# Optimization experiments

Measured on AMD Instinct MI355X. Metric: run time of the kernel, lower is better.

The kernel has to match this reference:

```python
import jax, jax.numpy as jnp
import numpy as np
from jax import lax

B, L, C, K = 32, 128, 192, 3


def conv1d_same(x, w, b):
    # x: [B, L, C], w: [K, Cin, Cout], b: [Cout]
    y = lax.conv_general_dilated(x, w, window_strides=(1,), padding='SAME',
                                 dimension_numbers=('NWC', 'WIO', 'NWC'))
    return y + b


def shift_right(x):
    # ShiftLayer: shift memory one step along length axis, zero-padded
    return jnp.pad(x, ((0, 0), (1, 0), (0, 0)))[:, :-1, :]


def setup_inputs() -> dict:
    key = jax.random.key(0)
    ks = jax.random.split(key, 4)
    scale = 1.0 / np.sqrt(K * C)
    x = jax.random.normal(ks[0], (B, L, C), dtype=jnp.float32)
    w_reset = jax.random.normal(ks[1], (K, C, C), dtype=jnp.float32) * scale
    w_gate = jax.random.normal(ks[2], (K, C, C), dtype=jnp.float32) * scale
    w_cand = jax.random.normal(ks[3], (K, C, C), dtype=jnp.float32) * scale
    b_reset = jnp.full((C,), 0.5, dtype=jnp.float32)  # bias_initializer 0.5
    b_gate = jnp.full((C,), 0.7, dtype=jnp.float32)   # bias_initializer 0.7
    b_cand = jnp.zeros((C,), dtype=jnp.float32)       # bias_initializer 0.0
    return {'x': x, 'w_reset': w_reset, 'b_reset': b_reset,
            'w_gate': w_gate, 'b_gate': b_gate,
            'w_cand': w_cand, 'b_cand': b_cand}


def reference(x, w_reset, b_reset, w_gate, b_gate, w_cand, b_cand):
    def step(mem, _):
        shifted = shift_right(mem)
        reset = jax.nn.sigmoid(conv1d_same(mem, w_reset, b_reset))
        gate = jax.nn.sigmoid(conv1d_same(mem, w_gate, b_gate))
        cand = jnp.tanh(conv1d_same(reset * mem, w_cand, b_cand))
        out = gate * shifted + (1.0 - gate) * cand
        return out, None

    # DNGPU unrolls the gated-conv cell for `length` (= seq_len) steps
    out, _ = lax.scan(step, x, None, length=L)
    return out
```

## Files before the change

### kernel.cpp

```cpp
#include <hip/hip_runtime.h>

typedef __attribute__((ext_vector_type(8))) short short8;
typedef __attribute__((ext_vector_type(4))) float f32x4;

#define NROWS 4096
#define CC    192
#define NCEL  (NROWS * CC)

#define W1ELEM (4 * 18 * 96 * 32)
#define W2ELEM (2 * 18 * 96 * 32)

typedef const __attribute__((address_space(1))) void as1_void;
typedef __attribute__((address_space(3))) void as3_void;
#define GLD_LDS16(G, L) __builtin_amdgcn_global_load_lds((as1_void*)(G), (as3_void*)(L), 16, 0, 0)

__device__ __forceinline__ unsigned short f2bf(float x) {
    union { float f; unsigned int u; } v; v.f = x;
    unsigned int r = v.u + 0x7fffu + ((v.u >> 16) & 1u);
    return (unsigned short)(r >> 16);
}
__device__ __forceinline__ float bf2f(unsigned short h) {
    union { unsigned int u; float f; } v; v.u = ((unsigned int)h) << 16;
    return v.f;
}
__device__ __forceinline__ unsigned packhl(float x) {
    unsigned short h = f2bf(x);
    unsigned short l = f2bf(x - bf2f(h));
    return (unsigned)h | ((unsigned)l << 16);
}
__device__ __forceinline__ float unpackhl(unsigned v) {
    return bf2f((unsigned short)(v & 0xFFFFu)) + bf2f((unsigned short)(v >> 16));
}
__device__ __forceinline__ float sigmoid_f(float x) {
    return 1.0f / (1.0f + __expf(-x));
}
__device__ __forceinline__ float tanh_f(float x) {
    float ax = fabsf(x);
    if (ax < 0.0625f) {
        float x2 = x * x;
        return x * fmaf(x2, fmaf(x2, 0.13333333f, -0.33333333f), 1.0f);
    }
    float e = __expf(2.0f * fminf(ax, 20.0f));
    float t = (e - 1.0f) / (e + 1.0f);
    return x < 0.0f ? -t : t;
}

__global__ void prep_x(const float* __restrict__ x, unsigned* __restrict__ memHL) {
    int i = blockIdx.x * 256 + threadIdx.x;
    if (i < NCEL) memHL[i] = packhl(x[i]);
}

__global__ void prep_w(const float* __restrict__ wr, const float* __restrict__ wg,
                       const float* __restrict__ wc,
                       unsigned short* __restrict__ W1H, unsigned short* __restrict__ W1L,
                       unsigned short* __restrict__ W2H, unsigned short* __restrict__ W2L) {
    int i = blockIdx.x * 256 + threadIdx.x;
    if (i >= W1ELEM + W2ELEM) return;
    const float* w; int grp, rem, cbase; unsigned short *H, *L; int dst;
    if (i < W1ELEM) {
        grp = i / 55296; rem = i % 55296;
        w = (grp >> 1) ? wg : wr;
        cbase = (grp & 1) * 96;
        H = W1H; L = W1L; dst = i;
    } else {
        int ii = i - W1ELEM;
        grp = ii / 55296; rem = ii % 55296;
        w = wc; cbase = grp * 96;
        H = W2H; L = W2L; dst = ii;
    }
    int ch = rem / 3072, r2 = rem % 3072, col = r2 / 32, kc = r2 % 32;
    int kk = ch / 6, ci = (ch % 6) * 32 + kc;
    int c = cbase + col;
    float v = w[(size_t)(kk * 192 + ci) * 192 + c];
    unsigned short h = f2bf(v);
    H[dst] = h; L[dst] = f2bf(v - bf2f(h));
}

#define ASTAGE(SRC, NT, NIT) do {                                                    \
    _Pragma("unroll")                                                                \
    for (int it_ = 0; it_ < (NIT); ++it_) {                                          \
        int q_ = it_ * (NT) + tid;                                                   \
        if (q_ < 34 * 96) {                                                          \
            int row_ = q_ / 96, u_ = q_ - row_ * 96;                                 \
            int gr_ = n0 - 1 + row_;                                                 \
            unsigned long long v_ = 0ull;                                            \
            if (gr_ >= 0 && ((gr_ >> 7) == (n0 >> 7)))                               \
                v_ = *(const unsigned long long*)((SRC) + (size_t)gr_ * 192 + u_ * 2);\
            unsigned lo_ = (unsigned)v_, hi_ = (unsigned)(v_ >> 32);                 \
            unsigned byt_ = ((unsigned)(u_ * 4)) ^ (((unsigned)(row_ & 7)) << 4);    \
            unsigned wdx_ = (((unsigned)row_) * 384 + byt_) >> 2;                    \
            ((unsigned*)AH)[wdx_] = (lo_ & 0xFFFFu) | (hi_ << 16);                   \
            ((unsigned*)AL)[wdx_] = (lo_ >> 16) | (hi_ & 0xFFFF0000u);               \
        }                                                                            \
    }                                                                                \
} while (0)

__global__ __launch_bounds__(128)
void k1_rg(const unsigned* __restrict__ mem,
           const unsigned short* __restrict__ W1H, const unsigned short* __restrict__ W1L,
           const float* __restrict__ b_r, const float* __restrict__ b_g,
           float* __restrict__ gate, unsigned* __restrict__ rm)
{
    __shared__ __align__(16) unsigned short AH[34 * 192];
    __shared__ __align__(16) unsigned short AL[34 * 192];
    __shared__ __align__(16) unsigned short WB[2][2][96 * 32];

    const int strip = blockIdx.x, grp = blockIdx.y;
    const int n0 = strip * 32;
    const int tid = threadIdx.x;

    ASTAGE(mem, 128, 26);

    const int lane = tid & 63, w = tid >> 6;
    const int lrow = lane & 15, lkg = lane >> 4;

    const unsigned short* Wp = (w ? W1L : W1H) + (size_t)grp * 55296;
    #define STAGEB1(BUF, CH) do {                                                    \
        const unsigned short* s_ = Wp + (CH) * 3072 + lane * 8;                      \
        unsigned short* d_ = &WB[BUF][w][0];                                         \
        _Pragma("unroll")                                                            \
        for (int j_ = 0; j_ < 6; ++j_)                                               \
            GLD_LDS16(s_ + j_ * 512, d_ + j_ * 512);                                 \
    } while (0)

    STAGEB1(0, 0);
    __syncthreads();

    f32x4 acc[2][3] = {};
    int buf = 0;
    #pragma unroll 2
    for (int ch = 0; ch < 18; ++ch) {
        if (ch < 17) STAGEB1(buf ^ 1, ch + 1);
        const int kk = ch / 6, cib = (ch % 6) * 32;
        short8 aH[2], aL[2];
        #pragma unroll
        for (int mt = 0; mt < 2; ++mt) {
            const int slot = 16 * mt + lrow + kk;
            const unsigned byt = ((unsigned)((cib + lkg * 8) * 2)) ^ (((unsigned)(slot & 7)) << 4);
            const int off = slot * 192 + (byt >> 1);
            aH[mt] = *(const short8*)(AH + off);
            aL[mt] = *(const short8*)(AL + off);
        }
        short8 bH[3], bL[3];
        #pragma unroll
        for (int j = 0; j < 3; ++j) {
            const int c = w * 48 + j * 16 + lrow;
            bH[j] = *(const short8*)(&WB[buf][0][c * 32 + lkg * 8]);
            bL[j] = *(const short8*)(&WB[buf][1][c * 32 + lkg * 8]);
        }
        #pragma unroll
        for (int mt = 0; mt < 2; ++mt)
            #pragma unroll
            for (int j = 0; j < 3; ++j) {
                acc[mt][j] = __builtin_amdgcn_mfma_f32_16x16x32_bf16(aH[mt], bH[j], acc[mt][j], 0, 0, 0);
                acc[mt][j] = __builtin_amdgcn_mfma_f32_16x16x32_bf16(aL[mt], bH[j], acc[mt][j], 0, 0, 0);
                acc[mt][j] = __builtin_amdgcn_mfma_f32_16x16x32_bf16(aH[mt], bL[j], acc[mt][j], 0, 0, 0);
            }
        __syncthreads();
        buf ^= 1;
    }

    const int conv = grp >> 1;
    const int c0g = (grp & 1) * 96 + w * 48;
    #pragma unroll
    for (int j = 0; j < 3; ++j) {
        const int c = c0g + 16 * j + lrow;
        const float bb = conv ? b_g[c] : b_r[c];
        #pragma unroll
        for (int mt = 0; mt < 2; ++mt) {
            #pragma unroll
            for (int r = 0; r < 4; ++r) {
                const int row = n0 + 16 * mt + lkg * 4 + r;
                const size_t idx = (size_t)row * 192 + c;
                const float s = sigmoid_f(acc[mt][j][r] + bb);
                if (conv == 0) {
                    const float m = unpackhl(mem[idx]);
                    rm[idx] = packhl(s * m);
                } else {
                    gate[idx] = s;
                }
            }
        }
    }
}

__global__ __launch_bounds__(256)
void k2_c(const unsigned* __restrict__ rm,
          const unsigned short* __restrict__ W2H, const unsigned short* __restrict__ W2L,
          const float* __restrict__ b_c, const float* __restrict__ gate,
          const unsigned* __restrict__ mem, unsigned* __restrict__ nxt,
          float* __restrict__ outF, int last)
{
    __shared__ __align__(16) unsigned short AH[34 * 192];
    __shared__ __align__(16) unsigned short AL[34 * 192];
    __shared__ __align__(16) unsigned short WB[2][2][96 * 32];

    const int strip = blockIdx.x, grp = blockIdx.y;
    const int n0 = strip * 32;
    const int tid = threadIdx.x;

    ASTAGE(rm, 256, 13);

    const int lane = tid & 63, w = tid >> 6;
    const int lrow = lane & 15, lkg = lane >> 4;
    const int mtw = w >> 1, ng = w & 1;

    const unsigned short* WpH = W2H + (size_t)grp * 55296;
    const unsigned short* WpL = W2L + (size_t)grp * 55296;
    #define STAGEB2(BUF, CH) do {                                                    \
        _Pragma("unroll")                                                            \
        for (int j_ = 0; j_ < 3; ++j_) {                                             \
            const int id_ = w * 3 + j_;                                              \
            const int pl_ = id_ / 6, sg_ = id_ % 6;                                  \
            const unsigned short* s_ = (pl_ ? WpL : WpH) + (CH) * 3072 + sg_ * 512 + lane * 8; \
            GLD_LDS16(s_, &WB[BUF][pl_][sg_ * 512]);                                 \
        }                                                                            \
    } while (0)

    STAGEB2(0, 0);
    __syncthreads();

    f32x4 acc[3] = {};
    int buf = 0;
    #pragma unroll 2
    for (int ch = 0; ch < 18; ++ch) {
        if (ch < 17) STAGEB2(buf ^ 1, ch + 1);
        const int kk = ch / 6, cib = (ch % 6) * 32;
        const int slot = 16 * mtw + lrow + kk;
        const unsigned byt = ((unsigned)((cib + lkg * 8) * 2)) ^ (((unsigned)(slot & 7)) << 4);
        const int off = slot * 192 + (byt >> 1);
        const short8 aH = *(const short8*)(AH + off);
        const short8 aL = *(const short8*)(AL + off);
        short8 bH[3], bL[3];
        #pragma unroll
        for (int j = 0; j < 3; ++j) {
            const int c = ng * 48 + j * 16 + lrow;
            bH[j] = *(const short8*)(&WB[buf][0][c * 32 + lkg * 8]);
            bL[j] = *(const short8*)(&WB[buf][1][c * 32 + lkg * 8]);
        }
        #pragma unroll
        for (int j = 0; j < 3; ++j) {
            acc[j] = __builtin_amdgcn_mfma_f32_16x16x32_bf16(aH, bH[j], acc[j], 0, 0, 0);
            acc[j] = __builtin_amdgcn_mfma_f32_16x16x32_bf16(aL, bH[j], acc[j], 0, 0, 0);
            acc[j] = __builtin_amdgcn_mfma_f32_16x16x32_bf16(aH, bL[j], acc[j], 0, 0, 0);
        }
        __syncthreads();
        buf ^= 1;
    }

    const int c0g = grp * 96 + ng * 48;
    #pragma unroll
    for (int j = 0; j < 3; ++j) {
        const int c = c0g + 16 * j + lrow;
        const float bcv = b_c[c];
        #pragma unroll
        for (int r = 0; r < 4; ++r) {
            const int row = n0 + 16 * mtw + lkg * 4 + r;
            const size_t idx = (size_t)row * 192 + c;
            const float cand = tanh_f(acc[j][r] + bcv);
            const float g = gate[idx];
            float sh = 0.0f;
            if (row & 127) sh = unpackhl(mem[idx - 192]);
            const float o = g * sh + (1.0f - g) * cand;
            if (last) outF[idx] = o;
            else      nxt[idx] = packhl(o);
        }
    }
}

extern "C" void kernel_launch(void* const* d_in, const int* in_sizes, int n_in,
                              void* d_out, int out_size, void* d_ws, size_t ws_size,
                              hipStream_t stream)
{
    (void)in_sizes; (void)n_in; (void)out_size; (void)ws_size;
    const float* x   = (const float*)d_in[0];
    const float* w_r = (const float*)d_in[1];
    const float* b_r = (const float*)d_in[2];
    const float* w_g = (const float*)d_in[3];
    const float* b_g = (const float*)d_in[4];
    const float* w_c = (const float*)d_in[5];
    const float* b_c = (const float*)d_in[6];
    float* out = (float*)d_out;

    const size_t NC = (size_t)NCEL;
    unsigned* mem0 = (unsigned*)d_ws;
    unsigned* mem1 = mem0 + NC;
    unsigned* rm   = mem1 + NC;
    float*    gate = (float*)(rm + NC);
    unsigned short* W1H = (unsigned short*)(gate + NC);
    unsigned short* W1L = W1H + (size_t)W1ELEM;
    unsigned short* W2H = W1L + (size_t)W1ELEM;
    unsigned short* W2L = W2H + (size_t)W2ELEM;

    prep_x<<<dim3((NCEL + 255) / 256), dim3(256), 0, stream>>>(x, mem0);
    prep_w<<<dim3((W1ELEM + W2ELEM + 255) / 256), dim3(256), 0, stream>>>(
        w_r, w_g, w_c, W1H, W1L, W2H, W2L);

    for (int t = 0; t < 128; ++t) {
        const unsigned* cur = (t & 1) ? mem1 : mem0;
        unsigned* nxt = (t & 1) ? mem0 : mem1;
        k1_rg<<<dim3(128, 4), dim3(128), 0, stream>>>(cur, W1H, W1L, b_r, b_g, gate, rm);
        k2_c<<<dim3(128, 2), dim3(256), 0, stream>>>(rm, W2H, W2L, b_c, gate,
                                                     cur, nxt, out, t == 127);
    }
}
```

Before: 4.269 ms.

## Switch reset/gate kernel to 32x32 MFMA with swizzled unified weight layout

The reset/gate kernel now runs 3 waves with one 32x32x16 bf16 MFMA tile each, instead of 2 waves issuing 16x16x32 tiles. Weights are repacked into a single buffer with hi/lo planes interleaved per chunk and a rotating slot swizzle, so B-operand LDS reads avoid bank conflicts and staging uses simple linear loads. The epilogue also reads the memory value for reset*mem from the LDS A tile rather than from global memory. Fewer but larger MFMAs and conflict-free B reads are meant to raise matrix-core throughput, at the cost of a changed thread count and more complex indexing.

```diff
diff --git a/kernel.cpp b/kernel.cpp
--- a/kernel.cpp
+++ b/kernel.cpp
@@ -1,14 +1,14 @@
 #include <hip/hip_runtime.h>
 
-typedef __attribute__((ext_vector_type(8))) short short8;
-typedef __attribute__((ext_vector_type(4))) float f32x4;
+typedef __attribute__((ext_vector_type(8)))  short short8;
+typedef __attribute__((ext_vector_type(4)))  float f32x4;
+typedef __attribute__((ext_vector_type(16))) float f32x16;
 
 #define NROWS 4096
 #define CC    192
 #define NCEL  (NROWS * CC)
 
-#define W1ELEM (4 * 18 * 96 * 32)
-#define W2ELEM (2 * 18 * 96 * 32)
+#define WTELEM (6 * 18 * 2 * 384 * 8)
 
 typedef const __attribute__((address_space(1))) void as1_void;
 typedef __attribute__((address_space(3))) void as3_void;
@@ -51,29 +51,26 @@
 }
 
 __global__ void prep_w(const float* __restrict__ wr, const float* __restrict__ wg,
-                       const float* __restrict__ wc,
-                       unsigned short* __restrict__ W1H, unsigned short* __restrict__ W1L,
-                       unsigned short* __restrict__ W2H, unsigned short* __restrict__ W2L) {
-    int i = blockIdx.x * 256 + threadIdx.x;
-    if (i >= W1ELEM + W2ELEM) return;
-    const float* w; int grp, rem, cbase; unsigned short *H, *L; int dst;
-    if (i < W1ELEM) {
-        grp = i / 55296; rem = i % 55296;
-        w = (grp >> 1) ? wg : wr;
-        cbase = (grp & 1) * 96;
-        H = W1H; L = W1L; dst = i;
-    } else {
-        int ii = i - W1ELEM;
-        grp = ii / 55296; rem = ii % 55296;
-        w = wc; cbase = grp * 96;
-        H = W2H; L = W2L; dst = ii;
-    }
-    int ch = rem / 3072, r2 = rem % 3072, col = r2 / 32, kc = r2 % 32;
-    int kk = ch / 6, ci = (ch % 6) * 32 + kc;
-    int c = cbase + col;
-    float v = w[(size_t)(kk * 192 + ci) * 192 + c];
+                       const float* __restrict__ wc, unsigned short* __restrict__ Wt) {
+    int o = blockIdx.x * 256 + threadIdx.x;
+    if (o >= WTELEM) return;
+    int e  = o & 7;
+    int b  = o >> 3;
+    int p  = b % 384;
+    int pl = (b / 384) % 2;
+    int ch = (b / 768) % 18;
+    int grp = b / (768 * 18);
+    int col = p >> 2;
+    int slotp = p & 3;
+    int slot = (slotp - col) & 3;
+    int kk = ch / 6;
+    int ci = (ch % 6) * 32 + slot * 8 + e;
+    int conv = grp >> 1;
+    int cglob = (grp & 1) * 96 + col;
+    const float* w = (conv == 0) ? wr : ((conv == 1) ? wg : wc);
+    float v = w[(size_t)(kk * 192 + ci) * 192 + cglob];
     unsigned short h = f2bf(v);
-    H[dst] = h; L[dst] = f2bf(v - bf2f(h));
+    Wt[o] = pl ? f2bf(v - bf2f(h)) : h;
 }
 
 #define ASTAGE(SRC, NT, NIT) do {                                                    \
@@ -95,107 +92,101 @@
     }                                                                                \
 } while (0)
 
-__global__ __launch_bounds__(128)
+#define STAGEB(BUF, CH, NT) do {                                                     \
+    const unsigned short* s_ = Wsec + (size_t)(CH) * 6144;                           \
+    _Pragma("unroll")                                                                \
+    for (int it_ = 0; it_ < 768 / (NT); ++it_) {                                     \
+        int q_ = it_ * (NT) + tid;                                                   \
+        GLD_LDS16(s_ + q_ * 8, &WB[BUF][q_ * 8]);                                    \
+    }                                                                                \
+} while (0)
+
+__global__ __launch_bounds__(192)
 void k1_rg(const unsigned* __restrict__ mem,
-           const unsigned short* __restrict__ W1H, const unsigned short* __restrict__ W1L,
+           const unsigned short* __restrict__ Wt,
            const float* __restrict__ b_r, const float* __restrict__ b_g,
            float* __restrict__ gate, unsigned* __restrict__ rm)
 {
     __shared__ __align__(16) unsigned short AH[34 * 192];
     __shared__ __align__(16) unsigned short AL[34 * 192];
-    __shared__ __align__(16) unsigned short WB[2][2][96 * 32];
+    __shared__ __align__(16) unsigned short WB[2][6144];
 
     const int strip = blockIdx.x, grp = blockIdx.y;
     const int n0 = strip * 32;
     const int tid = threadIdx.x;
 
-    ASTAGE(mem, 128, 26);
+    ASTAGE(mem, 192, 17);
 
     const int lane = tid & 63, w = tid >> 6;
-    const int lrow = lane & 15, lkg = lane >> 4;
-
-    const unsigned short* Wp = (w ? W1L : W1H) + (size_t)grp * 55296;
-    #define STAGEB1(BUF, CH) do {                                                    \
-        const unsigned short* s_ = Wp + (CH) * 3072 + lane * 8;                      \
-        unsigned short* d_ = &WB[BUF][w][0];                                         \
-        _Pragma("unroll")                                                            \
-        for (int j_ = 0; j_ < 6; ++j_)                                               \
-            GLD_LDS16(s_ + j_ * 512, d_ + j_ * 512);                                 \
-    } while (0)
-
-    STAGEB1(0, 0);
+    const int lr32 = lane & 31, khalf = lane >> 5;
+    const int col96 = w * 32 + lr32;
+
+    const unsigned short* Wsec = Wt + (size_t)grp * 18 * 6144;
+
+    STAGEB(0, 0, 192);
     __syncthreads();
 
-    f32x4 acc[2][3] = {};
+    f32x16 acc = {};
     int buf = 0;
     #pragma unroll 2
     for (int ch = 0; ch < 18; ++ch) {
-        if (ch < 17) STAGEB1(buf ^ 1, ch + 1);
-        const int kk = ch / 6, cib = (ch % 6) * 32;
-        short8 aH[2], aL[2];
-        #pragma unroll
-        for (int mt = 0; mt < 2; ++mt) {
-            const int slot = 16 * mt + lrow + kk;
-            const unsigned byt = ((unsigned)((cib + lkg * 8) * 2)) ^ (((unsigned)(slot & 7)) << 4);
-            const int off = slot * 192 + (byt >> 1);
-            aH[mt] = *(const short8*)(AH + off);
-            aL[mt] = *(const short8*)(AL + off);
-        }
-        short8 bH[3], bL[3];
-        #pragma unroll
-        for (int j = 0; j < 3; ++j) {
-            const int c = w * 48 + j * 16 + lrow;
-            bH[j] = *(const short8*)(&WB[buf][0][c * 32 + lkg * 8]);
-            bL[j] = *(const short8*)(&WB[buf][1][c * 32 + lkg * 8]);
-        }
-        #pragma unroll
-        for (int mt = 0; mt < 2; ++mt)
-            #pragma unroll
-            for (int j = 0; j < 3; ++j) {
-                acc[mt][j] = __builtin_amdgcn_mfma_f32_16x16x32_bf16(aH[mt], bH[j], acc[mt][j], 0, 0, 0);
-                acc[mt][j] = __builtin_amdgcn_mfma_f32_16x16x32_bf16(aL[mt], bH[j], acc[mt][j], 0, 0, 0);
-                acc[mt][j] = __builtin_amdgcn_mfma_f32_16x16x32_bf16(aH[mt], bL[j], acc[mt][j], 0, 0, 0);
-            }
+        if (ch < 17) STAGEB(buf ^ 1, ch + 1, 192);
+        const int kk = ch / 6, ci0 = (ch % 6) * 32;
+        const int tr = lr32 + kk;
+        short8 aH[2], aL[2], bH[2], bL[2];
+        #pragma unroll
+        for (int ks = 0; ks < 2; ++ks) {
+            const int slot = ks * 2 + khalf;
+            const unsigned byt = ((unsigned)((ci0 + slot * 8) * 2)) ^ (((unsigned)(tr & 7)) << 4);
+            const int aoff = tr * 192 + (byt >> 1);
+            aH[ks] = *(const short8*)(AH + aoff);
+            aL[ks] = *(const short8*)(AL + aoff);
+            const int boff = col96 * 32 + ((slot + col96) & 3) * 8;
+            bH[ks] = *(const short8*)(&WB[buf][boff]);
+            bL[ks] = *(const short8*)(&WB[buf][3072 + boff]);
+        }
+        #pragma unroll
+        for (int ks = 0; ks < 2; ++ks) {
+            acc = __builtin_amdgcn_mfma_f32_32x32x16_bf16(aH[ks], bH[ks], acc, 0, 0, 0);
+            acc = __builtin_amdgcn_mfma_f32_32x32x16_bf16(aL[ks], bH[ks], acc, 0, 0, 0);
+            acc = __builtin_amdgcn_mfma_f32_32x32x16_bf16(aH[ks], bL[ks], acc, 0, 0, 0);
+        }
         __syncthreads();
         buf ^= 1;
     }
 
     const int conv = grp >> 1;
-    const int c0g = (grp & 1) * 96 + w * 48;
+    const int chan = (grp & 1) * 96 + col96;
+    const float bb = conv ? b_g[chan] : b_r[chan];
     #pragma unroll
-    for (int j = 0; j < 3; ++j) {
-        const int c = c0g + 16 * j + lrow;
-        const float bb = conv ? b_g[c] : b_r[c];
-        #pragma unroll
-        for (int mt = 0; mt < 2; ++mt) {
-            #pragma unroll
-            for (int r = 0; r < 4; ++r) {
-                const int row = n0 + 16 * mt + lkg * 4 + r;
-                const size_t idx = (size_t)row * 192 + c;
-                const float s = sigmoid_f(acc[mt][j][r] + bb);
-                if (conv == 0) {
-                    const float m = unpackhl(mem[idx]);
-                    rm[idx] = packhl(s * m);
-                } else {
-                    gate[idx] = s;
-                }
-            }
+    for (int r = 0; r < 16; ++r) {
+        const int rl = (r & 3) + 8 * (r >> 2) + 4 * khalf;
+        const int row = n0 + rl;
+        const size_t idx = (size_t)row * 192 + chan;
+        const float s = sigmoid_f(acc[r] + bb);
+        if (conv == 0) {
+            const int tr = rl + 1;
+            const unsigned sb = ((unsigned)(chan * 2)) ^ (((unsigned)(tr & 7)) << 4);
+            const float m = bf2f(AH[tr * 192 + (sb >> 1)]) + bf2f(AL[tr * 192 + (sb >> 1)]);
+            rm[idx] = packhl(s * m);
+        } else {
+            gate[idx] = s;
         }
     }
 }
 
 __global__ __launch_bounds__(256)
 void k2_c(const unsigned* __restrict__ rm,
-          const unsigned short* __restrict__ W2H, const unsigned short* __restrict__ W2L,
+          const unsigned short* __restrict__ Wt,
           const float* __restrict__ b_c, const float* __restrict__ gate,
           const unsigned* __restrict__ mem, unsigned* __restrict__ nxt,
           float* __restrict__ outF, int last)
 {
     __shared__ __align__(16) unsigned short AH[34 * 192];
     __shared__ __align__(16) unsigned short AL[34 * 192];
-    __shared__ __align__(16) unsigned short WB[2][2][96 * 32];
-
-    const int strip = blockIdx.x, grp = blockIdx.y;
+    __shared__ __align__(16) unsigned short WB[2][6144];
+
+    const int strip = blockIdx.x, half = blockIdx.y;
     const int n0 = strip * 32;
     const int tid = threadIdx.x;
 
@@ -205,38 +196,29 @@
     const int lrow = lane & 15, lkg = lane >> 4;
     const int mtw = w >> 1, ng = w & 1;
 
-    const unsigned short* WpH = W2H + (size_t)grp * 55296;
-    const unsigned short* WpL = W2L + (size_t)grp * 55296;
-    #define STAGEB2(BUF, CH) do {                                                    \
-        _Pragma("unroll")                                                            \
-        for (int j_ = 0; j_ < 3; ++j_) {                                             \
-            const int id_ = w * 3 + j_;                                              \
-            const int pl_ = id_ / 6, sg_ = id_ % 6;                                  \
-            const unsigned short* s_ = (pl_ ? WpL : WpH) + (CH) * 3072 + sg_ * 512 + lane * 8; \
-            GLD_LDS16(s_, &WB[BUF][pl_][sg_ * 512]);                                 \
-        }                                                                            \
-    } while (0)
-
-    STAGEB2(0, 0);
+    const unsigned short* Wsec = Wt + (size_t)(4 + half) * 18 * 6144;
+
+    STAGEB(0, 0, 256);
     __syncthreads();
 
     f32x4 acc[3] = {};
     int buf = 0;
     #pragma unroll 2
     for (int ch = 0; ch < 18; ++ch) {
-        if (ch < 17) STAGEB2(buf ^ 1, ch + 1);
-        const int kk = ch / 6, cib = (ch % 6) * 32;
-        const int slot = 16 * mtw + lrow + kk;
-        const unsigned byt = ((unsigned)((cib + lkg * 8) * 2)) ^ (((unsigned)(slot & 7)) << 4);
-        const int off = slot * 192 + (byt >> 1);
-        const short8 aH = *(const short8*)(AH + off);
-        const short8 aL = *(const short8*)(AL + off);
+        if (ch < 17) STAGEB(buf ^ 1, ch + 1, 256);
+        const int kk = ch / 6, ci0 = (ch % 6) * 32;
+        const int tr = 16 * mtw + lrow + kk;
+        const unsigned byt = ((unsigned)((ci0 + lkg * 8) * 2)) ^ (((unsigned)(tr & 7)) << 4);
+        const int aoff = tr * 192 + (byt >> 1);
+        const short8 aH = *(const short8*)(AH + aoff);
+        const short8 aL = *(const short8*)(AL + aoff);
         short8 bH[3], bL[3];
         #pragma unroll
         for (int j = 0; j < 3; ++j) {
-            const int c = ng * 48 + j * 16 + lrow;
-            bH[j] = *(const short8*)(&WB[buf][0][c * 32 + lkg * 8]);
-            bL[j] = *(const short8*)(&WB[buf][1][c * 32 + lkg * 8]);
+            const int c96 = ng * 48 + j * 16 + lrow;
+            const int boff = c96 * 32 + ((lkg + c96) & 3) * 8;
+            bH[j] = *(const short8*)(&WB[buf][boff]);
+            bL[j] = *(const short8*)(&WB[buf][3072 + boff]);
         }
         #pragma unroll
         for (int j = 0; j < 3; ++j) {
@@ -248,15 +230,14 @@
         buf ^= 1;
     }
 
-    const int c0g = grp * 96 + ng * 48;
     #pragma unroll
     for (int j = 0; j < 3; ++j) {
-        const int c = c0g + 16 * j + lrow;
-        const float bcv = b_c[c];
+        const int chan = half * 96 + ng * 48 + j * 16 + lrow;
+        const float bcv = b_c[chan];
         #pragma unroll
         for (int r = 0; r < 4; ++r) {
             const int row = n0 + 16 * mtw + lkg * 4 + r;
-            const size_t idx = (size_t)row * 192 + c;
+            const size_t idx = (size_t)row * 192 + chan;
             const float cand = tanh_f(acc[j][r] + bcv);
             const float g = gate[idx];
             float sh = 0.0f;
@@ -287,20 +268,16 @@
     unsigned* mem1 = mem0 + NC;
     unsigned* rm   = mem1 + NC;
     float*    gate = (float*)(rm + NC);
-    unsigned short* W1H = (unsigned short*)(gate + NC);
-    unsigned short* W1L = W1H + (size_t)W1ELEM;
-    unsigned short* W2H = W1L + (size_t)W1ELEM;
-    unsigned short* W2L = W2H + (size_t)W2ELEM;
+    unsigned short* Wt = (unsigned short*)(gate + NC);
 
     prep_x<<<dim3((NCEL + 255) / 256), dim3(256), 0, stream>>>(x, mem0);
-    prep_w<<<dim3((W1ELEM + W2ELEM + 255) / 256), dim3(256), 0, stream>>>(
-        w_r, w_g, w_c, W1H, W1L, W2H, W2L);
+    prep_w<<<dim3((WTELEM + 255) / 256), dim3(256), 0, stream>>>(w_r, w_g, w_c, Wt);
 
     for (int t = 0; t < 128; ++t) {
         const unsigned* cur = (t & 1) ? mem1 : mem0;
         unsigned* nxt = (t & 1) ? mem0 : mem1;
-        k1_rg<<<dim3(128, 4), dim3(128), 0, stream>>>(cur, W1H, W1L, b_r, b_g, gate, rm);
-        k2_c<<<dim3(128, 2), dim3(256), 0, stream>>>(rm, W2H, W2L, b_c, gate,
+        k1_rg<<<dim3(128, 4), dim3(192), 0, stream>>>(cur, Wt, b_r, b_g, gate, rm);
+        k2_c<<<dim3(128, 2), dim3(256), 0, stream>>>(rm, Wt, b_c, gate,
                                                      cur, nxt, out, t == 127);
     }
 }
```

After: 3.798 ms. -11.0%, faster.
